# Performance work log

Measured on AMD Instinct MI355X. Metric: run time of the kernel, lower is better.

Reference implementation:

```python
import jax, jax.numpy as jnp
import numpy as np

P = 8  # hard-coded patch size in DCTFFN

def dct_matrix(n):
    # get_dctMatrix: orthonormal DCT-II basis
    j = np.arange(n)
    i = np.arange(n).reshape(-1, 1)
    C = np.cos(np.pi * i * (2 * j + 1) / (2 * n)) * np.sqrt(2.0 / n)
    C[0, :] = np.sqrt(1.0 / n)
    return jnp.asarray(C, dtype=jnp.float32)

def setup_inputs():
    key = jax.random.key(0)
    ks = jax.random.split(key, 4)
    dim, hidden = 64, 170
    x = jax.random.normal(ks[0], (4, dim, 256, 256), jnp.float32)
    W_in = jax.random.normal(ks[1], (2 * hidden, dim), jnp.float32) * 0.05
    W_dw = jax.random.normal(ks[2], (2 * hidden, 1, 3, 3), jnp.float32) * 0.1
    quant = jnp.ones((2 * hidden, 1, 1, P, P), jnp.float32)
    W_out = jax.random.normal(ks[3], (dim, hidden), jnp.float32) * 0.05
    return dict(x=x, W_in=W_in, W_dw=W_dw, quant=quant, W_out=W_out)

def reference(x, W_in, W_dw, quant, W_out):
    M = dct_matrix(P)  # [8,8], used for both H and W axes (patch is square)
    # project_in: 1x1 conv, no bias
    y = jnp.einsum('oc,bchw->bohw', W_in, x)
    b, c2, h, w = y.shape
    ph = (P - h % P) % P
    pw = (P - w % P) % P
    if ph or pw:
        y = jnp.pad(y, ((0, 0), (0, 0), (0, ph), (0, pw)), mode='reflect')
    H, W = y.shape[-2:]
    # b c (h p1) (w p2) -> b c h w p1 p2
    xp = y.reshape(b, c2, H // P, P, W // P, P).transpose(0, 1, 2, 4, 3, 5)
    # 2D DCT per 8x8 patch: Y = M @ X @ M^T
    xd = jnp.einsum('ip,bchwpq,jq->bchwij', M, xp, M)
    xd = xd * quant  # learned frequency scaling, broadcast over (h, w)
    # 2D IDCT: Y = M^T @ X @ M
    xi = jnp.einsum('pi,bchwpq,qj->bchwij', M, xd, M)
    # back to b c H W, crop padding
    yr = xi.transpose(0, 1, 2, 4, 3, 5).reshape(b, c2, H, W)[:, :, :h, :w]
    # depthwise 3x3 conv, padding=1, no bias
    dw = jax.lax.conv_general_dilated(
        yr, W_dw, window_strides=(1, 1), padding=((1, 1), (1, 1)),
        dimension_numbers=('NCHW', 'OIHW', 'NCHW'), feature_group_count=c2)
    x1, x2 = jnp.split(dw, 2, axis=1)
    g = jax.nn.gelu(x1, approximate=False) * x2
    # project_out: 1x1 conv, no bias
    return jnp.einsum('oc,bchw->bohw', W_out, g)
```

## Files before the change

kernel.cpp:

```cpp
#include <hip/hip_runtime.h>
#include <cmath>

#define HW   256
#define NPIX 65536
#define NP   65600
#define CIN  64
#define C2   340
#define HID  170

typedef _Float16 f16x8 __attribute__((ext_vector_type(8)));
typedef float    f32x4 __attribute__((ext_vector_type(4)));

#define A0 0.35355339059327373f
#define A1 0.49039264020161522f
#define A2 0.46193976625564337f
#define A3 0.41573480615127262f
#define A4 0.35355339059327379f
#define A5 0.27778511650980114f
#define A6 0.19134171618254492f
#define A7 0.09754516100806417f

__device__ __forceinline__ void dct8(const float v[8], float y[8]) {
    const float u0 = v[0] + v[7], u1 = v[1] + v[6];
    const float u2 = v[2] + v[5], u3 = v[3] + v[4];
    const float w0 = v[0] - v[7], w1 = v[1] - v[6];
    const float w2 = v[2] - v[5], w3 = v[3] - v[4];
    const float s0 = u0 + u3, s1 = u1 + u2;
    const float t0 = u0 - u3, t1 = u1 - u2;
    y[0] = A0 * (s0 + s1);
    y[4] = A4 * (s0 - s1);
    y[2] = fmaf(A2, t0,  A6 * t1);
    y[6] = fmaf(A6, t0, -A2 * t1);
    y[1] = fmaf(A1, w0, fmaf( A3, w1, fmaf( A5, w2,  A7 * w3)));
    y[3] = fmaf(A3, w0, fmaf(-A7, w1, fmaf(-A1, w2, -A5 * w3)));
    y[5] = fmaf(A5, w0, fmaf(-A1, w1, fmaf( A7, w2,  A3 * w3)));
    y[7] = fmaf(A7, w0, fmaf(-A5, w1, fmaf( A3, w2, -A1 * w3)));
}

__device__ __forceinline__ void idct8(const float y[8], float x[8]) {
    const float sa = fmaf( A4, y[4], A0 * y[0]);
    const float sb = fmaf(-A4, y[4], A0 * y[0]);
    const float c0 = fmaf( A2, y[2],  A6 * y[6]);
    const float c1 = fmaf( A6, y[2], -A2 * y[6]);
    const float e0 = sa + c0, e3 = sa - c0;
    const float e1 = sb + c1, e2 = sb - c1;
    const float o0 = fmaf(A1, y[1], fmaf( A3, y[3], fmaf( A5, y[5],  A7 * y[7])));
    const float o1 = fmaf(A3, y[1], fmaf(-A7, y[3], fmaf(-A1, y[5], -A5 * y[7])));
    const float o2 = fmaf(A5, y[1], fmaf(-A1, y[3], fmaf( A7, y[5],  A3 * y[7])));
    const float o3 = fmaf(A7, y[1], fmaf(-A5, y[3], fmaf( A3, y[5], -A1 * y[7])));
    x[0] = e0 + o0; x[7] = e0 - o0;
    x[1] = e1 + o1; x[6] = e1 - o1;
    x[2] = e2 + o2; x[5] = e2 - o2;
    x[3] = e3 + o3; x[4] = e3 - o3;
}

__device__ __forceinline__ int pcolrot(int blk, int row, int ocl) {
    return ((blk + row + (ocl >> 2)) & 3) << 3;
}

__global__ __launch_bounds__(256) void kprep(const float* __restrict__ Win,
                                             const float* __restrict__ Wout,
                                             _Float16* __restrict__ WinH,
                                             _Float16* __restrict__ WoutKH)
{
    const int i = blockIdx.x * 256 + threadIdx.x;
    if (i < 352 * 64) WinH[i] = (i < C2 * 64) ? (_Float16)Win[i] : (_Float16)0.f;
    if (i < 64 * 192) {
        const int o = i / 192, h = i - o * 192;
        WoutKH[i] = (h < HID) ? (_Float16)Wout[o * HID + h] : (_Float16)0.f;
    }
}

__global__ __launch_bounds__(256) void kA(
    const float* __restrict__ x,
    const _Float16* __restrict__ WinH,
    const float* __restrict__ quant,
    _Float16* __restrict__ yr)
{
    const int tid  = threadIdx.x;
    const int tile = blockIdx.x;
    const int bb   = blockIdx.y;
    const int ty = tile >> 3, tx = tile & 7;
    const int y0 = ty * 8,    x0 = tx * 32;
    const int r  = tid >> 5,  c  = tid & 31;
    const int wv = tid >> 6;
    const int l15 = tid & 15, quad = (tid & 63) >> 4;

    __shared__ union {
        _Float16 ash[256 * 64];
        float    csh[32 * 264];
    } shm;

    if (tile == 0) {
        const f16x8 z = {(_Float16)0.f,(_Float16)0.f,(_Float16)0.f,(_Float16)0.f,
                         (_Float16)0.f,(_Float16)0.f,(_Float16)0.f,(_Float16)0.f};
#pragma unroll 1
        for (int it = 0; it < 11; ++it) {
            const int idx = tid + it * 256;
            if (idx < C2 * 8) {
                const int oc = idx >> 3, sub = idx & 7;
                *(f16x8*)&yr[(size_t)(bb * C2 + oc) * NP + NPIX + sub * 8] = z;
            }
        }
    }

    const float* xp = x + (size_t)bb * (CIN * NPIX) + (y0 + r) * HW + (x0 + c);
    const int sw = tid & 7;
#pragma unroll
    for (int u = 0; u < 8; ++u) {
        union { _Float16 h[8]; f16x8 v; } pk;
#pragma unroll
        for (int j = 0; j < 8; ++j) pk.h[j] = (_Float16)xp[(size_t)(u * 8 + j) * NPIX];
        *(f16x8*)&shm.ash[tid * 64 + ((u ^ sw) * 8)] = pk.v;
    }
    __syncthreads();

    f16x8 af0[4], af1[4];
#pragma unroll
    for (int tt = 0; tt < 4; ++tt) {
        const int apx = (wv * 4 + tt) * 16 + l15;
        const int asw = apx & 7;
        af0[tt] = *(const f16x8*)&shm.ash[apx * 64 + ((quad ^ asw) * 8)];
        af1[tt] = *(const f16x8*)&shm.ash[apx * 64 + (((4 + quad) ^ asw) * 8)];
    }
    __syncthreads();

    const int ch  = tid >> 5;
    const int pat = (tid >> 3) & 3;
    const int lan = tid & 7;

#pragma unroll 1
    for (int sc = 0; sc < 11; ++sc) {
        const int oc0 = sc * 32;

#pragma unroll
        for (int g2 = 0; g2 < 2; ++g2) {
            const int ocb = oc0 + g2 * 16 + l15;
            const f16x8 b0 = *(const f16x8*)(WinH + ocb * 64 + quad * 8);
            const f16x8 b1 = *(const f16x8*)(WinH + ocb * 64 + 32 + quad * 8);
#pragma unroll
            for (int tt = 0; tt < 4; ++tt) {
                const int tile16 = wv * 4 + tt;
                f32x4 acc = {0.f, 0.f, 0.f, 0.f};
                acc = __builtin_amdgcn_mfma_f32_16x16x32_f16(af0[tt], b0, acc, 0, 0, 0);
                acc = __builtin_amdgcn_mfma_f32_16x16x32_f16(af1[tt], b1, acc, 0, 0, 0);
                const int ocl = g2 * 16 + l15;
                const int prow = tile16 >> 1;
                const int blk  = ((tile16 & 1) << 1) | (quad >> 1);
                *(f32x4*)&shm.csh[ocl * 264 + prow * 32 + pcolrot(blk, prow, ocl)
                                  + (quad & 1) * 4] = acc;
            }
        }
        __syncthreads();

#pragma unroll
        for (int di = 0; di < 4; ++di) {
            const int ocl = ch + 8 * di;
            float* row = &shm.csh[ocl * 264 + lan * 32 + pcolrot(pat, lan, ocl)];
            float v[8], o[8];
            *(f32x4*)&v[0] = *(const f32x4*)row;
            *(f32x4*)&v[4] = *(const f32x4*)(row + 4);
            dct8(v, o);
            *(f32x4*)row       = *(const f32x4*)&o[0];
            *(f32x4*)(row + 4) = *(const f32x4*)&o[4];
        }
        __syncthreads();

#pragma unroll
        for (int di = 0; di < 4; ++di) {
            const int ocl = ch + 8 * di;
            float v[8], d[8], e[8];
#pragma unroll
            for (int i = 0; i < 8; ++i)
                v[i] = shm.csh[ocl * 264 + i * 32 + pcolrot(pat, i, ocl) + lan];
            int ocq = oc0 + ocl; if (ocq > C2 - 1) ocq = C2 - 1;
            const float* qp = quant + ocq * 64 + lan;
            dct8(v, d);
#pragma unroll
            for (int i = 0; i < 8; ++i) d[i] *= qp[i * 8];
            idct8(d, e);
#pragma unroll
            for (int i = 0; i < 8; ++i)
                shm.csh[ocl * 264 + i * 32 + pcolrot(pat, i, ocl) + lan] = e[i];
        }
        __syncthreads();

#pragma unroll
        for (int di = 0; di < 4; ++di) {
            const int ocl = ch + 8 * di;
            const int oc  = oc0 + ocl;
            const float* row = &shm.csh[ocl * 264 + lan * 32 + pcolrot(pat, lan, ocl)];
            float v[8], e[8];
            *(f32x4*)&v[0] = *(const f32x4*)row;
            *(f32x4*)&v[4] = *(const f32x4*)(row + 4);
            idct8(v, e);
            union { _Float16 h[8]; f16x8 f; } u;
#pragma unroll
            for (int q = 0; q < 8; ++q) u.h[q] = (_Float16)e[q];
            if (oc < C2) {
                f16x8* dst = (f16x8*)(yr + (size_t)(bb * C2 + oc) * NP
                                      + (y0 + lan) * HW + x0 + pat * 8);
                *dst = u.f;
            }
        }
        __syncthreads();
    }
}

__global__ __launch_bounds__(256, 2) void kB(
    const _Float16* __restrict__ yr,
    const float* __restrict__ Wdw,
    const _Float16* __restrict__ WoutKH,
    float* __restrict__ out)
{
    const int tid = threadIdx.x;
    const int bb  = blockIdx.y;
    const int id  = blockIdx.x;
    const int row = ((id & 7) << 5) | (id >> 3);
    const int wv  = tid >> 6;
    const int L   = tid & 63;
    const int l15 = tid & 15, quad = (tid & 63) >> 4;

    __shared__ union {
        _Float16 g[256 * 32];
        float    t[16 * 257];
    } shm;

    const char* ybase = (const char*)(yr + (size_t)bb * C2 * NP) - 16;

    unsigned boff[3];
#pragma unroll
    for (int rr = 0; rr < 3; ++rr) {
        const int trow = row + rr - 1;
        boff[rr] = ((unsigned)trow < (unsigned)HW)
                 ? (unsigned)(trow * (HW * 2) + 8 * L + 12)
                 : (unsigned)(NPIX * 2 + 16);
    }
    const float mL = (L == 0)  ? 0.f : 1.f;
    const float mR = (L == 63) ? 0.f : 1.f;

    f32x4 acc[4][4];
#pragma unroll
    for (int a = 0; a < 4; ++a)
#pragma unroll
        for (int b = 0; b < 4; ++b) acc[a][b] = (f32x4){0.f, 0.f, 0.f, 0.f};

    char* gpc = (char*)shm.g + L * 256 + ((wv ^ (L & 3)) << 4);

#pragma unroll 1
    for (int chunk = 0; chunk < 6; ++chunk) {
        const int hc = chunk * 32;

        union { _Float16 h[8]; f16x8 v; } pk0, pk1, pk2, pk3;
#pragma unroll
        for (int j = 0; j < 8; ++j) {
            const int h = hc + wv * 8 + j;
            float gg0 = 0.f, gg1 = 0.f, gg2 = 0.f, gg3 = 0.f;
            if (h < HID) {
                const char* p1 = ybase + (size_t)h * (NP * 2);
                const char* p2 = p1 + (size_t)HID * (NP * 2);
                const float* w1 = Wdw + h * 9;
                const float* w2 = w1 + HID * 9;
                float s1[4] = {0.f, 0.f, 0.f, 0.f};
                float s2[4] = {0.f, 0.f, 0.f, 0.f};
#pragma unroll
                for (int rr = 0; rr < 3; ++rr) {
                    f16x8 a1, a2;
                    __builtin_memcpy(&a1, p1 + boff[rr], 16);
                    __builtin_memcpy(&a2, p2 + boff[rr], 16);
                    float v1[8], v2[8];
#pragma unroll
                    for (int e = 1; e <= 6; ++e) {
                        v1[e] = (float)a1[e];
                        v2[e] = (float)a2[e];
                    }
                    v1[1] *= mL; v2[1] *= mL;
                    v1[6] *= mR; v2[6] *= mR;
                    const float wa = w1[rr*3+0], wb = w1[rr*3+1], wc = w1[rr*3+2];
                    const float wd = w2[rr*3+0], we = w2[rr*3+1], wf = w2[rr*3+2];
#pragma unroll
                    for (int i = 0; i < 4; ++i) {
                        s1[i] = fmaf(v1[i+1], wa, s1[i]);
                        s1[i] = fmaf(v1[i+2], wb, s1[i]);
                        s1[i] = fmaf(v1[i+3], wc, s1[i]);
                        s2[i] = fmaf(v2[i+1], wd, s2[i]);
                        s2[i] = fmaf(v2[i+2], we, s2[i]);
                        s2[i] = fmaf(v2[i+3], wf, s2[i]);
                    }
                }
                const float KC = 0.70710678118654752f;
                gg0 = 0.5f * s1[0] * (1.f + erff(s1[0] * KC)) * s2[0];
                gg1 = 0.5f * s1[1] * (1.f + erff(s1[1] * KC)) * s2[1];
                gg2 = 0.5f * s1[2] * (1.f + erff(s1[2] * KC)) * s2[2];
                gg3 = 0.5f * s1[3] * (1.f + erff(s1[3] * KC)) * s2[3];
            }
            pk0.h[j] = (_Float16)gg0;
            pk1.h[j] = (_Float16)gg1;
            pk2.h[j] = (_Float16)gg2;
            pk3.h[j] = (_Float16)gg3;
        }
        *(f16x8*)(gpc      ) = pk0.v;
        *(f16x8*)(gpc +  64) = pk1.v;
        *(f16x8*)(gpc + 128) = pk2.v;
        *(f16x8*)(gpc + 192) = pk3.v;
        __syncthreads();

#pragma unroll
        for (int tt = 0; tt < 4; ++tt) {
            const int apx = (wv * 4 + tt) * 16 + l15;
            const f16x8 a = *(const f16x8*)((const char*)shm.g + apx * 64
                              + ((quad ^ ((l15 >> 2) & 3)) << 4));
#pragma unroll
            for (int p = 0; p < 4; ++p) {
                const f16x8 b = *(const f16x8*)(WoutKH + (p * 16 + l15) * 192 + hc + quad * 8);
                acc[tt][p] = __builtin_amdgcn_mfma_f32_16x16x32_f16(a, b, acc[tt][p], 0, 0, 0);
            }
        }
        __syncthreads();
    }

    float* ob = out + (size_t)bb * CIN * NPIX + row * HW + tid;
#pragma unroll
    for (int p = 0; p < 4; ++p) {
#pragma unroll
        for (int tt = 0; tt < 4; ++tt) {
            const int px = (wv * 4 + tt) * 16 + quad * 4;
#pragma unroll
            for (int reg = 0; reg < 4; ++reg)
                shm.t[l15 * 257 + px + reg] = acc[tt][p][reg];
        }
        __syncthreads();
#pragma unroll
        for (int o2 = 0; o2 < 16; ++o2)
            ob[(size_t)(p * 16 + o2) * NPIX] = shm.t[o2 * 257 + tid];
        __syncthreads();
    }
}

extern "C" void kernel_launch(void* const* d_in, const int* in_sizes, int n_in,
                              void* d_out, int out_size, void* d_ws, size_t ws_size,
                              hipStream_t stream)
{
    const float* x     = (const float*)d_in[0];
    const float* Win   = (const float*)d_in[1];
    const float* Wdw   = (const float*)d_in[2];
    const float* quant = (const float*)d_in[3];
    const float* Wout  = (const float*)d_in[4];
    float* out = (float*)d_out;

    _Float16* WinH   = (_Float16*)d_ws;
    _Float16* WoutKH = (_Float16*)((char*)d_ws + 45056);
    _Float16* yrbuf  = (_Float16*)((char*)d_ws + 69632);

    const size_t perBatch = (size_t)C2 * NP * sizeof(_Float16);
    const size_t head = 69632;
    const size_t avail = ws_size > head ? ws_size - head : 0;
    int nb = 1;
    if (avail >= 4 * perBatch)      nb = 4;
    else if (avail >= 2 * perBatch) nb = 2;

    kprep<<<88, 256, 0, stream>>>(Win, Wout, WinH, WoutKH);

    for (int b0 = 0; b0 < 4; b0 += nb) {
        dim3 grid(256, nb);
        kA<<<grid, 256, 0, stream>>>(x + (size_t)b0 * CIN * NPIX, WinH, quant, yrbuf);
        kB<<<grid, 256, 0, stream>>>(yrbuf, Wdw, WoutKH, out + (size_t)b0 * CIN * NPIX);
    }
}
```

Measured before the change: 332.2 us.

## Apply forward DCT to input channels before projection to skip per-output DCT

```diff
diff --git a/kernel.cpp b/kernel.cpp
--- a/kernel.cpp
+++ b/kernel.cpp
@@ -82,14 +82,10 @@
     const int bb   = blockIdx.y;
     const int ty = tile >> 3, tx = tile & 7;
     const int y0 = ty * 8,    x0 = tx * 32;
-    const int r  = tid >> 5,  c  = tid & 31;
     const int wv = tid >> 6;
     const int l15 = tid & 15, quad = (tid & 63) >> 4;
 
-    __shared__ union {
-        _Float16 ash[256 * 64];
-        float    csh[32 * 264];
-    } shm;
+    __shared__ float csh[32 * 264];
 
     if (tile == 0) {
         const f16x8 z = {(_Float16)0.f,(_Float16)0.f,(_Float16)0.f,(_Float16)0.f,
@@ -104,30 +100,59 @@
         }
     }
 
-    const float* xp = x + (size_t)bb * (CIN * NPIX) + (y0 + r) * HW + (x0 + c);
-    const int sw = tid & 7;
-#pragma unroll
-    for (int u = 0; u < 8; ++u) {
-        union { _Float16 h[8]; f16x8 v; } pk;
-#pragma unroll
-        for (int j = 0; j < 8; ++j) pk.h[j] = (_Float16)xp[(size_t)(u * 8 + j) * NPIX];
-        *(f16x8*)&shm.ash[tid * 64 + ((u ^ sw) * 8)] = pk.v;
-    }
-    __syncthreads();
-
-    f16x8 af0[4], af1[4];
-#pragma unroll
-    for (int tt = 0; tt < 4; ++tt) {
-        const int apx = (wv * 4 + tt) * 16 + l15;
-        const int asw = apx & 7;
-        af0[tt] = *(const f16x8*)&shm.ash[apx * 64 + ((quad ^ asw) * 8)];
-        af1[tt] = *(const f16x8*)&shm.ash[apx * 64 + (((4 + quad) ^ asw) * 8)];
-    }
-    __syncthreads();
-
     const int ch  = tid >> 5;
     const int pat = (tid >> 3) & 3;
     const int lan = tid & 7;
+
+    const float* xb = x + (size_t)bb * (CIN * NPIX);
+
+    f16x8 af0[4], af1[4];
+#pragma unroll
+    for (int hh = 0; hh < 2; ++hh) {
+#pragma unroll
+        for (int di = 0; di < 4; ++di) {
+            const int ci = ch + 8 * di;
+            const float* gp = xb + (size_t)(hh * 32 + ci) * NPIX
+                              + (y0 + lan) * HW + x0 + pat * 8;
+            float v[8], o[8];
+            *(f32x4*)&v[0] = *(const f32x4*)gp;
+            *(f32x4*)&v[4] = *(const f32x4*)(gp + 4);
+            dct8(v, o);
+            float* rowp = &csh[ci * 264 + lan * 32 + pcolrot(pat, lan, ci)];
+            *(f32x4*)rowp       = *(const f32x4*)&o[0];
+            *(f32x4*)(rowp + 4) = *(const f32x4*)&o[4];
+        }
+        __syncthreads();
+#pragma unroll
+        for (int di = 0; di < 4; ++di) {
+            const int ci = ch + 8 * di;
+            float v[8], o[8];
+#pragma unroll
+            for (int i = 0; i < 8; ++i)
+                v[i] = csh[ci * 264 + i * 32 + pcolrot(pat, i, ci) + lan];
+            dct8(v, o);
+#pragma unroll
+            for (int i = 0; i < 8; ++i)
+                csh[ci * 264 + i * 32 + pcolrot(pat, i, ci) + lan] = o[i];
+        }
+        __syncthreads();
+#pragma unroll
+        for (int tt = 0; tt < 4; ++tt) {
+            const int apx = (wv * 4 + tt) * 16 + l15;
+            const int prw = apx >> 5;
+            const int pc  = apx & 31;
+            const int pp  = pc >> 3, pl = pc & 7;
+            union { _Float16 h[8]; f16x8 v; } pk;
+#pragma unroll
+            for (int e = 0; e < 8; ++e) {
+                const int ci = quad * 8 + e;
+                pk.h[e] = (_Float16)csh[ci * 264 + prw * 32
+                                        + pcolrot(pp, prw, ci) + pl];
+            }
+            if (hh == 0) af0[tt] = pk.v; else af1[tt] = pk.v;
+        }
+        __syncthreads();
+    }
 
 #pragma unroll 1
     for (int sc = 0; sc < 11; ++sc) {
@@ -138,17 +163,21 @@
             const int ocb = oc0 + g2 * 16 + l15;
             const f16x8 b0 = *(const f16x8*)(WinH + ocb * 64 + quad * 8);
             const f16x8 b1 = *(const f16x8*)(WinH + ocb * 64 + 32 + quad * 8);
+            const int ocl = g2 * 16 + l15;
+            int ocq = oc0 + ocl; if (ocq > C2 - 1) ocq = C2 - 1;
+            const float* qbase = quant + ocq * 64 + (quad & 1) * 4;
 #pragma unroll
             for (int tt = 0; tt < 4; ++tt) {
                 const int tile16 = wv * 4 + tt;
                 f32x4 acc = {0.f, 0.f, 0.f, 0.f};
                 acc = __builtin_amdgcn_mfma_f32_16x16x32_f16(af0[tt], b0, acc, 0, 0, 0);
                 acc = __builtin_amdgcn_mfma_f32_16x16x32_f16(af1[tt], b1, acc, 0, 0, 0);
-                const int ocl = g2 * 16 + l15;
                 const int prow = tile16 >> 1;
                 const int blk  = ((tile16 & 1) << 1) | (quad >> 1);
-                *(f32x4*)&shm.csh[ocl * 264 + prow * 32 + pcolrot(blk, prow, ocl)
-                                  + (quad & 1) * 4] = acc;
+                const f32x4 qv = *(const f32x4*)(qbase + prow * 8);
+                acc *= qv;
+                *(f32x4*)&csh[ocl * 264 + prow * 32 + pcolrot(blk, prow, ocl)
+                              + (quad & 1) * 4] = acc;
             }
         }
         __syncthreads();
@@ -156,32 +185,14 @@
 #pragma unroll
         for (int di = 0; di < 4; ++di) {
             const int ocl = ch + 8 * di;
-            float* row = &shm.csh[ocl * 264 + lan * 32 + pcolrot(pat, lan, ocl)];
-            float v[8], o[8];
-            *(f32x4*)&v[0] = *(const f32x4*)row;
-            *(f32x4*)&v[4] = *(const f32x4*)(row + 4);
-            dct8(v, o);
-            *(f32x4*)row       = *(const f32x4*)&o[0];
-            *(f32x4*)(row + 4) = *(const f32x4*)&o[4];
-        }
-        __syncthreads();
-
-#pragma unroll
-        for (int di = 0; di < 4; ++di) {
-            const int ocl = ch + 8 * di;
-            float v[8], d[8], e[8];
+            float v[8], e8[8];
 #pragma unroll
             for (int i = 0; i < 8; ++i)
-                v[i] = shm.csh[ocl * 264 + i * 32 + pcolrot(pat, i, ocl) + lan];
-            int ocq = oc0 + ocl; if (ocq > C2 - 1) ocq = C2 - 1;
-            const float* qp = quant + ocq * 64 + lan;
-            dct8(v, d);
-#pragma unroll
-            for (int i = 0; i < 8; ++i) d[i] *= qp[i * 8];
-            idct8(d, e);
+                v[i] = csh[ocl * 264 + i * 32 + pcolrot(pat, i, ocl) + lan];
+            idct8(v, e8);
 #pragma unroll
             for (int i = 0; i < 8; ++i)
-                shm.csh[ocl * 264 + i * 32 + pcolrot(pat, i, ocl) + lan] = e[i];
+                csh[ocl * 264 + i * 32 + pcolrot(pat, i, ocl) + lan] = e8[i];
         }
         __syncthreads();
 
@@ -189,14 +200,14 @@
         for (int di = 0; di < 4; ++di) {
             const int ocl = ch + 8 * di;
             const int oc  = oc0 + ocl;
-            const float* row = &shm.csh[ocl * 264 + lan * 32 + pcolrot(pat, lan, ocl)];
-            float v[8], e[8];
-            *(f32x4*)&v[0] = *(const f32x4*)row;
-            *(f32x4*)&v[4] = *(const f32x4*)(row + 4);
-            idct8(v, e);
+            const float* rowp = &csh[ocl * 264 + lan * 32 + pcolrot(pat, lan, ocl)];
+            float v[8], e8[8];
+            *(f32x4*)&v[0] = *(const f32x4*)rowp;
+            *(f32x4*)&v[4] = *(const f32x4*)(rowp + 4);
+            idct8(v, e8);
             union { _Float16 h[8]; f16x8 f; } u;
 #pragma unroll
-            for (int q = 0; q < 8; ++q) u.h[q] = (_Float16)e[q];
+            for (int q = 0; q < 8; ++q) u.h[q] = (_Float16)e8[q];
             if (oc < C2) {
                 f16x8* dst = (f16x8*)(yr + (size_t)(bb * C2 + oc) * NP
                                       + (y0 + lan) * HW + x0 + pat * 8);
```

Measured after the change: 308.4 us. 7.2% less time.
